# Optimization experiments

Measured on AMD Instinct MI355X. Metric: run time of the kernel, lower is better.

## Reference

```python
import jax, jax.numpy as jnp
import numpy as np

WS, WS2, UP = 8, 16, 2
DIM, HEADS = 192, 6
HD = DIM // HEADS
SCALE = HD ** -0.5
EPS = 1e-5

def _rel_index():
    r1, c1 = np.meshgrid(np.arange(WS), np.arange(WS), indexing='ij')
    r2, c2 = np.meshgrid(np.arange(WS2), np.arange(WS2), indexing='ij')
    r1, c1 = r1.ravel(), c1.ravel()          # 64 query positions
    r2, c2 = r2.ravel(), c2.ravel()          # 256 kv positions
    rel_row = r1[:, None] - r2[None, :]
    rel_col = c1[:, None] - c2[None, :]
    off = WS * UP - 1    # 15
    span = WS + WS * UP - 1  # 23
    return jnp.asarray((rel_row + off) * span + (rel_col + off))  # (64, 256)

REL_IDX = _rel_index()

def layer_norm(x, w, b):
    m = x.mean(-1, keepdims=True)
    v = ((x - m) ** 2).mean(-1, keepdims=True)
    return (x - m) * jax.lax.rsqrt(v + EPS) * w + b

def window_partition(x, ws):
    B, H, W, C = x.shape
    x = x.reshape(B, H // ws, ws, W // ws, ws, C).transpose(0, 1, 3, 2, 4, 5)
    return x.reshape(-1, ws * ws, C)

def window_reverse(w, ws, H, W, B):
    x = w.reshape(B, H // ws, W // ws, ws, ws, -1).transpose(0, 1, 3, 2, 4, 5)
    return x.reshape(B, H, W, -1)

def setup_inputs() -> dict:
    key = jax.random.key(0)
    ks = jax.random.split(key, 8)
    B, H, W, H2, W2 = 4, 128, 128, 256, 256
    s = 0.02
    return {
        'x': jax.random.normal(ks[0], (B, H * W, DIM), jnp.float32),
        'x2': jax.random.normal(ks[1], (B, H2 * W2, DIM), jnp.float32),
        'norm1_w': jnp.ones((DIM,), jnp.float32),
        'norm1_b': jnp.zeros((DIM,), jnp.float32),
        'qkv_w': jax.random.normal(ks[2], (DIM, DIM), jnp.float32) * s,
        'qkv_b': jnp.zeros((DIM,), jnp.float32),
        'qkv2_w': jax.random.normal(ks[3], (2 * DIM, DIM), jnp.float32) * s,
        'qkv2_b': jnp.zeros((2 * DIM,), jnp.float32),
        'rel_bias': jax.random.normal(ks[4], (23 * 23, HEADS), jnp.float32) * s,
        'proj_w': jax.random.normal(ks[5], (DIM, DIM), jnp.float32) * s,
        'proj_b': jnp.zeros((DIM,), jnp.float32),
        'norm2_w': jnp.ones((DIM,), jnp.float32),
        'norm2_b': jnp.zeros((DIM,), jnp.float32),
        'fc1_w': jax.random.normal(ks[6], (4 * DIM, DIM), jnp.float32) * s,
        'fc1_b': jnp.zeros((4 * DIM,), jnp.float32),
        'fc2_w': jax.random.normal(ks[7], (DIM, 4 * DIM), jnp.float32) * s,
        'fc2_b': jnp.zeros((DIM,), jnp.float32),
        'H': 128, 'W': 128, 'H2': 256, 'W2': 256,
    }

def reference(x, x2, norm1_w, norm1_b, qkv_w, qkv_b, qkv2_w, qkv2_b, rel_bias,
              proj_w, proj_b, norm2_w, norm2_b, fc1_w, fc1_b, fc2_w, fc2_b,
              H, W, H2, W2):
    B, L, C = x.shape
    shortcut = x
    xn = layer_norm(x, norm1_w, norm1_b).reshape(B, H, W, C)
    x2r = x2.reshape(B, H2, W2, C)

    xw = window_partition(xn, WS)      # (nW, 64, C)
    x2w = window_partition(x2r, WS2)   # (nW, 256, C)

    q = (xw @ qkv_w.T + qkv_b).reshape(-1, WS * WS, HEADS, HD).transpose(0, 2, 1, 3)
    kv = (x2w @ qkv2_w.T + qkv2_b).reshape(-1, WS2 * WS2, 2, HEADS, HD).transpose(2, 0, 3, 1, 4)
    k, v = kv[0], kv[1]                # (nW, h, 256, d)

    attn = jnp.einsum('whnd,whmd->whnm', q * SCALE, k)   # (nW, h, 64, 256)
    bias = rel_bias[REL_IDX]                             # (64, 256, h)
    attn = attn + bias.transpose(2, 0, 1)[None]
    attn = jax.nn.softmax(attn, axis=-1)
    out = jnp.einsum('whnm,whmd->wnhd', attn, v).reshape(-1, WS * WS, C)
    out = out @ proj_w.T + proj_b

    x = shortcut + window_reverse(out, WS, H, W, B).reshape(B, H * W, C)
    h = layer_norm(x, norm2_w, norm2_b)
    h = jax.nn.gelu(h @ fc1_w.T + fc1_b, approximate=False)
    x = x + (h @ fc2_w.T + fc2_b)
    return x
```

## Files before the change

### kernel.cpp

```cpp
#include <hip/hip_runtime.h>
#include <hip/hip_bf16.h>
#include <math.h>

typedef unsigned int u32;
typedef unsigned short u16;

typedef __attribute__((ext_vector_type(8))) short bf16x8;
typedef __attribute__((ext_vector_type(4))) float f32x4;

__device__ __forceinline__ float bflo(u32 u){ union{u32 i; float f;} c; c.i = u << 16; return c.f; }
__device__ __forceinline__ float bfhi(u32 u){ union{u32 i; float f;} c; c.i = u & 0xffff0000u; return c.f; }
__device__ __forceinline__ float bfs(u16 s){ union{u32 i; float f;} c; c.i = ((u32)s) << 16; return c.f; }
__device__ __forceinline__ u32 packbf(float a, float b){
  union{float f; u32 i;} ca, cb; ca.f = a; cb.f = b;
  u32 ua = (ca.i + 0x7fffu + ((ca.i >> 16) & 1u)) >> 16;
  u32 ub = (cb.i + 0x7fffu + ((cb.i >> 16) & 1u)) >> 16;
  return (ua & 0xffffu) | (ub << 16);
}
__device__ __forceinline__ u16 bf1(float a){
  union{float f; u32 i;} c; c.f = a;
  return (u16)((c.i + 0x7fffu + ((c.i >> 16) & 1u)) >> 16);
}
__device__ __forceinline__ bf16x8 pack8(float f0,float f1,float f2,float f3,
                                        float f4,float f5,float f6,float f7){
  union { u32 u[4]; bf16x8 v; } cv;
  cv.u[0]=packbf(f0,f1); cv.u[1]=packbf(f2,f3); cv.u[2]=packbf(f4,f5); cv.u[3]=packbf(f6,f7);
  return cv.v;
}
__device__ __forceinline__ float gelu_exact(float v){ return 0.5f*v*(1.0f + erff(v*0.70710678118654752f)); }
__device__ __forceinline__ bool detect_f32(const u32* rawn1){ return (rawn1[0] & 0xFFFFu) == 0u; }

#define SCALE_Q 0.17677669529663687f

#define P_N1W 0
#define P_N1B 192
#define P_N2W 384
#define P_N2B 576
#define P_QKVB 768
#define P_QKV2B 960
#define P_PROJB 1344
#define P_FC1B 1536
#define P_FC2B 2304
#define P_RELB 2496
#define P_TOTAL 5670
#define W_QKV 0
#define W_QKV2 18432
#define W_PROJ 55296
#define W_FC1 73728
#define W_FC2 147456
#define W_TOTAL 221184

__device__ __forceinline__ void stage_w64x192(const u32* __restrict__ src, u32* lds, int tid){
  #pragma unroll
  for (int t = 0; t < 3; ++t) {
    int idx = tid + t*512;
    int j = idx / 24, seg = idx % 24;
    uint4 v = *(const uint4*)(src + (size_t)j*96 + seg*4);
    int byt = (j*384 + seg*16) ^ ((j&7)<<4);
    *(uint4*)((char*)lds + byt) = v;
  }
}
__device__ __forceinline__ void stage_w192x64(const u32* __restrict__ src, int ch, u32* lds, int tid){
  #pragma unroll
  for (int t = 0; t < 3; ++t) {
    int idx = tid + t*512;
    int j = idx / 8, seg = idx % 8;
    uint4 v = *(const uint4*)(src + (size_t)j*384 + ch*32 + seg*4);
    int byt = (j*128 + seg*16) ^ ((j&7)<<4);
    *(uint4*)((char*)lds + byt) = v;
  }
}
__device__ __forceinline__ bf16x8 lds_w64(const u32* lds, int j, int kt, int g){
  int byt = (j*384 + kt*64 + g*16) ^ ((j&7)<<4);
  return *(const bf16x8*)((const char*)lds + byt);
}
__device__ __forceinline__ bf16x8 lds_w192(const u32* lds, int j, int kk, int g){
  int byt = (j*128 + kk*64 + g*16) ^ ((j&7)<<4);
  return *(const bf16x8*)((const char*)lds + byt);
}

__global__ __launch_bounds__(256) void k_canon_w(
    const void* qkvw, const void* qkv2w, const void* projw,
    const void* fc1w, const void* fc2w, const u32* rawn1, u32* cw)
{
  int idx = blockIdx.x*256 + threadIdx.x;
  bool isf32 = detect_f32(rawn1);
  const void* src; int off;
  if      (idx < W_QKV2){ src=qkvw;  off=idx; }
  else if (idx < W_PROJ){ src=qkv2w; off=idx-W_QKV2; }
  else if (idx < W_FC1) { src=projw; off=idx-W_PROJ; }
  else if (idx < W_FC2) { src=fc1w;  off=idx-W_FC1; }
  else                  { src=fc2w;  off=idx-W_FC2; }
  u32 o;
  if (isf32) { float2 v = ((const float2*)src)[off]; o = packbf(v.x, v.y); }
  else       { o = ((const u32*)src)[off]; }
  cw[idx] = o;
}

__global__ __launch_bounds__(256) void k_canon_v(
    const void* n1w, const void* n1b, const void* n2w, const void* n2b,
    const void* qkvb, const void* qkv2b, const void* projb,
    const void* fc1b, const void* fc2b, const void* relb,
    const u32* rawn1, float* par)
{
  int idx = blockIdx.x*256 + threadIdx.x;
  if (idx >= P_TOTAL) return;
  bool isf32 = detect_f32(rawn1);
  const void* src; int off;
  if      (idx < P_N1B)  { src=n1w;  off=idx; }
  else if (idx < P_N2W)  { src=n1b;  off=idx-P_N1B; }
  else if (idx < P_N2B)  { src=n2w;  off=idx-P_N2W; }
  else if (idx < P_QKVB) { src=n2b;  off=idx-P_N2B; }
  else if (idx < P_QKV2B){ src=qkvb; off=idx-P_QKVB; }
  else if (idx < P_PROJB){ src=qkv2b;off=idx-P_QKV2B; }
  else if (idx < P_FC1B) { src=projb;off=idx-P_PROJB; }
  else if (idx < P_FC2B) { src=fc1b; off=idx-P_FC1B; }
  else if (idx < P_RELB) { src=fc2b; off=idx-P_FC2B; }
  else                   { src=relb; off=idx-P_RELB; }
  par[idx] = isf32 ? ((const float*)src)[off] : bfs(((const u16*)src)[off]);
}

__global__ __launch_bounds__(256) void k_bias(
    const float* __restrict__ par, float* __restrict__ tbl)
{
  int idx = blockIdx.x*256 + threadIdx.x;
  int h  = idx >> 12;
  int remi = idx & 4095;
  int kt = remi >> 8;
  int qt = (remi >> 6) & 3;
  int ll = idx & 63;
  int lr = ll & 15, g = ll >> 4;
  int q = qt*16 + lr;
  int r1 = q >> 3, c1 = q & 7;
  float vv[4];
  #pragma unroll
  for (int i = 0; i < 4; ++i) {
    int kv = kt*16 + 4*g + i;
    int r2 = kv >> 4, c2 = kv & 15;
    vv[i] = par[P_RELB + ((r1-r2+15)*23 + (c1-c2+15))*6 + h];
  }
  ((float4*)tbl)[idx] = make_float4(vv[0], vv[1], vv[2], vv[3]);
}

__global__ __launch_bounds__(512) void k_qproj(
    const void* __restrict__ x, const u32* __restrict__ rawn1,
    const u32* __restrict__ cw, const float* __restrict__ par,
    float* __restrict__ q_ws)
{
  __shared__ u32 wbuf[6144];
  int tid = threadIdx.x;
  int l = tid & 63, w = tid >> 6, lr = l & 15, g = l >> 4;
  int wi0 = blockIdx.x*4;
  bool isf32 = detect_f32(rawn1);

  bf16x8 a[2][6];
  #pragma unroll
  for (int mt = 0; mt < 2; ++mt) {
    int tb = w*32 + mt*16 + lr;
    int wi = wi0 + (tb >> 6);
    int t = tb & 63;
    int b = wi >> 8, rem = wi & 255, wh = rem >> 4, ww = rem & 15;
    int r = t >> 3, c = t & 7;
    size_t grow = (size_t)b*16384 + (size_t)(wh*8+r)*128 + (ww*8+c);
    float4 xf[12];
    if (isf32) {
      const float* xp = (const float*)x + grow*192;
      #pragma unroll
      for (int kt = 0; kt < 6; ++kt) {
        xf[kt*2]   = *(const float4*)(xp + kt*32 + 8*g);
        xf[kt*2+1] = *(const float4*)(xp + kt*32 + 8*g + 4);
      }
    } else {
      const u32* xp = (const u32*)x + grow*96;
      #pragma unroll
      for (int kt = 0; kt < 6; ++kt) {
        uint4 u = *(const uint4*)(xp + kt*16 + 4*g);
        xf[kt*2]   = make_float4(bflo(u.x), bfhi(u.x), bflo(u.y), bfhi(u.y));
        xf[kt*2+1] = make_float4(bflo(u.z), bfhi(u.z), bflo(u.w), bfhi(u.w));
      }
    }
    float s = 0.f, s2 = 0.f;
    #pragma unroll
    for (int q8 = 0; q8 < 12; ++q8) {
      s  += xf[q8].x + xf[q8].y + xf[q8].z + xf[q8].w;
      s2 += xf[q8].x*xf[q8].x + xf[q8].y*xf[q8].y + xf[q8].z*xf[q8].z + xf[q8].w*xf[q8].w;
    }
    s += __shfl_xor(s, 16); s2 += __shfl_xor(s2, 16);
    s += __shfl_xor(s, 32); s2 += __shfl_xor(s2, 32);
    float m = s * (1.f/192.f);
    float rstd = rsqrtf(s2*(1.f/192.f) - m*m + 1e-5f);
    #pragma unroll
    for (int kt = 0; kt < 6; ++kt) {
      int k0 = kt*32 + 8*g;
      float4 w0 = *(const float4*)(par + P_N1W + k0);
      float4 w1 = *(const float4*)(par + P_N1W + k0 + 4);
      float4 b0 = *(const float4*)(par + P_N1B + k0);
      float4 b1 = *(const float4*)(par + P_N1B + k0 + 4);
      float4 f0 = xf[kt*2], f1 = xf[kt*2+1];
      a[mt][kt] = pack8((f0.x-m)*rstd*w0.x + b0.x, (f0.y-m)*rstd*w0.y + b0.y,
                        (f0.z-m)*rstd*w0.z + b0.z, (f0.w-m)*rstd*w0.w + b0.w,
                        (f1.x-m)*rstd*w1.x + b1.x, (f1.y-m)*rstd*w1.y + b1.y,
                        (f1.z-m)*rstd*w1.z + b1.z, (f1.w-m)*rstd*w1.w + b1.w);
    }
  }

  for (int ch = 0; ch < 3; ++ch) {
    __syncthreads();
    stage_w64x192(cw + W_QKV + (size_t)(ch*64)*96, wbuf, tid);
    __syncthreads();
    #pragma unroll
    for (int nt2 = 0; nt2 < 4; ++nt2) {
      int j = ch*64 + nt2*16 + lr;
      f32x4 acc0 = {0.f,0.f,0.f,0.f}, acc1 = {0.f,0.f,0.f,0.f};
      #pragma unroll
      for (int kt = 0; kt < 6; ++kt) {
        bf16x8 bb = lds_w64(wbuf, nt2*16 + lr, kt, g);
        acc0 = __builtin_amdgcn_mfma_f32_16x16x32_bf16(a[0][kt], bb, acc0, 0, 0, 0);
        acc1 = __builtin_amdgcn_mfma_f32_16x16x32_bf16(a[1][kt], bb, acc1, 0, 0, 0);
      }
      float bj = par[P_QKVB + j];
      int h = j >> 5, d = j & 31;
      #pragma unroll
      for (int mt = 0; mt < 2; ++mt) {
        f32x4 acc = mt ? acc1 : acc0;
        #pragma unroll
        for (int i = 0; i < 4; ++i) {
          int tb = w*32 + mt*16 + 4*g + i;
          int wi = wi0 + (tb >> 6);
          int n = tb & 63;
          q_ws[(size_t)(wi*6+h)*2048 + (size_t)n*32 + d] = (acc[i] + bj) * SCALE_Q;
        }
      }
    }
  }
}

__global__ __launch_bounds__(512) void k_kvproj(
    const void* __restrict__ x2, const u32* __restrict__ rawn1,
    const u32* __restrict__ cw, const float* __restrict__ par,
    u16* __restrict__ k_ws, u16* __restrict__ v_ws, int win0)
{
  __shared__ u32 wbuf[6144];
  int tid = threadIdx.x;
  int l = tid & 63, w = tid >> 6, lr = l & 15, g = l >> 4;
  int lwi = blockIdx.x;
  int wi = win0 + lwi;
  int b = wi >> 8, rem = wi & 255, wh = rem >> 4, ww = rem & 15;
  bool isf32 = detect_f32(rawn1);

  bf16x8 a[2][6];
  #pragma unroll
  for (int mt = 0; mt < 2; ++mt) {
    int tt = w*32 + mt*16 + lr;
    int r = tt >> 4, c = tt & 15;
    size_t grow = (size_t)b*65536 + (size_t)(wh*16+r)*256 + (ww*16+c);
    if (isf32) {
      const float4* xp = (const float4*)x2 + grow*48;
      #pragma unroll
      for (int kt = 0; kt < 6; ++kt) {
        float4 f0 = xp[kt*8 + g*2];
        float4 f1 = xp[kt*8 + g*2 + 1];
        a[mt][kt] = pack8(f0.x,f0.y,f0.z,f0.w, f1.x,f1.y,f1.z,f1.w);
      }
    } else {
      const u32* xp = (const u32*)x2 + grow*96;
      #pragma unroll
      for (int kt = 0; kt < 6; ++kt)
        a[mt][kt] = *(const bf16x8*)(xp + kt*16 + g*4);
    }
  }

  for (int ch = 0; ch < 6; ++ch) {
    __syncthreads();
    stage_w64x192(cw + W_QKV2 + (size_t)(ch*64)*96, wbuf, tid);
    __syncthreads();
    if (ch < 3) {
      #pragma unroll
      for (int nt2 = 0; nt2 < 4; ++nt2) {
        int j = ch*64 + nt2*16 + lr;
        f32x4 acc0 = {0.f,0.f,0.f,0.f}, acc1 = {0.f,0.f,0.f,0.f};
        #pragma unroll
        for (int kt = 0; kt < 6; ++kt) {
          bf16x8 bb = lds_w64(wbuf, nt2*16 + lr, kt, g);
          acc0 = __builtin_amdgcn_mfma_f32_16x16x32_bf16(a[0][kt], bb, acc0, 0, 0, 0);
          acc1 = __builtin_amdgcn_mfma_f32_16x16x32_bf16(a[1][kt], bb, acc1, 0, 0, 0);
        }
        float bj = par[P_QKV2B + j];
        int h = j >> 5, d = j & 31;
        u16* dst = k_ws + (size_t)(lwi*6 + h)*8192 + d;
        #pragma unroll
        for (int mt = 0; mt < 2; ++mt) {
          f32x4 acc = mt ? acc1 : acc0;
          #pragma unroll
          for (int i = 0; i < 4; ++i) {
            int tok = w*32 + mt*16 + 4*g + i;
            dst[(size_t)tok*32] = bf1(acc[i] + bj);
          }
        }
      }
    } else {
      #pragma unroll
      for (int nt2 = 0; nt2 < 4; ++nt2) {
        f32x4 acc0 = {0.f,0.f,0.f,0.f}, acc1 = {0.f,0.f,0.f,0.f};
        #pragma unroll
        for (int kt = 0; kt < 6; ++kt) {
          bf16x8 bb = lds_w64(wbuf, nt2*16 + lr, kt, g);
          acc0 = __builtin_amdgcn_mfma_f32_16x16x32_bf16(bb, a[0][kt], acc0, 0, 0, 0);
          acc1 = __builtin_amdgcn_mfma_f32_16x16x32_bf16(bb, a[1][kt], acc1, 0, 0, 0);
        }
        int jr0 = (ch-3)*64 + nt2*16 + 4*g;
        #pragma unroll
        for (int mt = 0; mt < 2; ++mt) {
          f32x4 acc = mt ? acc1 : acc0;
          int tok = w*32 + mt*16 + lr;
          #pragma unroll
          for (int i = 0; i < 4; ++i) {
            int jp = jr0 + i;
            int h = jp >> 5, dd = jp & 31;
            v_ws[(size_t)(lwi*6 + h)*8192 + (size_t)dd*256 + tok] = bf1(acc[i] + par[P_QKV2B + 192 + jp]);
          }
        }
      }
    }
  }
}

__global__ __launch_bounds__(256) void k_attn(
    const float* __restrict__ q_ws, const u16* __restrict__ k_ws,
    const u16* __restrict__ v_ws, const float* __restrict__ tbl,
    u16* __restrict__ O_ws, int win0)
{
  __shared__ u32 Psh[4*64*16];
  int tid = threadIdx.x;
  int w = tid >> 6, l = tid & 63;
  int lr = l & 15, g = l >> 4;
  int task = blockIdx.x*4 + w;
  int lwi = task / 6, h = task - lwi*6;
  int wi = win0 + lwi;

  bf16x8 qb[4];
  {
    const float* qp = q_ws + (size_t)(wi*6+h)*2048;
    #pragma unroll
    for (int qt = 0; qt < 4; ++qt) {
      const float* qr = qp + (qt*16 + lr)*32 + 8*g;
      float4 f0 = *(const float4*)qr;
      float4 f1 = *(const float4*)(qr + 4);
      qb[qt] = pack8(f0.x,f0.y,f0.z,f0.w, f1.x,f1.y,f1.z,f1.w);
    }
  }
  const u16* kp = k_ws + (size_t)(lwi*6+h)*8192;
  const u16* vp = v_ws + (size_t)(lwi*6+h)*8192;
  const float4* tb4 = (const float4*)tbl + (size_t)h*4096 + l;

  f32x4 ao[2][4];
  #pragma unroll
  for (int dt = 0; dt < 2; ++dt)
    #pragma unroll
    for (int qt = 0; qt < 4; ++qt) ao[dt][qt] = (f32x4){0.f,0.f,0.f,0.f};
  float mreg[4] = {-3.0e38f,-3.0e38f,-3.0e38f,-3.0e38f};
  float sreg[4] = {0.f,0.f,0.f,0.f};
  u32* pbu = Psh + w*1024;

  for (int ch = 0; ch < 8; ++ch) {
    bf16x8 ka0 = *(const bf16x8*)(kp + (2*ch)*512   + lr*32 + 8*g);
    bf16x8 ka1 = *(const bf16x8*)(kp + (2*ch+1)*512 + lr*32 + 8*g);
    f32x4 s0[4], s1[4];
    #pragma unroll
    for (int qt = 0; qt < 4; ++qt) {
      float4 b0 = tb4[(2*ch)*256   + qt*64];
      float4 b1 = tb4[(2*ch+1)*256 + qt*64];
      f32x4 c0; c0[0]=b0.x; c0[1]=b0.y; c0[2]=b0.z; c0[3]=b0.w;
      f32x4 c1; c1[0]=b1.x; c1[1]=b1.y; c1[2]=b1.z; c1[3]=b1.w;
      s0[qt] = __builtin_amdgcn_mfma_f32_16x16x32_bf16(ka0, qb[qt], c0, 0, 0, 0);
      s1[qt] = __builtin_amdgcn_mfma_f32_16x16x32_bf16(ka1, qb[qt], c1, 0, 0, 0);
    }
    #pragma unroll
    for (int qt = 0; qt < 4; ++qt) {
      float pm = fmaxf(fmaxf(fmaxf(s0[qt][0],s0[qt][1]), fmaxf(s0[qt][2],s0[qt][3])),
                       fmaxf(fmaxf(s1[qt][0],s1[qt][1]), fmaxf(s1[qt][2],s1[qt][3])));
      pm = fmaxf(pm, __shfl_xor(pm, 16));
      pm = fmaxf(pm, __shfl_xor(pm, 32));
      float nm = fmaxf(mreg[qt], pm);
      float resc = __expf(mreg[qt] - nm);
      mreg[qt] = nm;
      float p00 = __expf(s0[qt][0]-nm), p01 = __expf(s0[qt][1]-nm),
            p02 = __expf(s0[qt][2]-nm), p03 = __expf(s0[qt][3]-nm);
      float p10 = __expf(s1[qt][0]-nm), p11 = __expf(s1[qt][1]-nm),
            p12 = __expf(s1[qt][2]-nm), p13 = __expf(s1[qt][3]-nm);
      float ps = ((p00+p01)+(p02+p03)) + ((p10+p11)+(p12+p13));
      ps += __shfl_xor(ps, 16);
      ps += __shfl_xor(ps, 32);
      sreg[qt] = sreg[qt]*resc + ps;
      #pragma unroll
      for (int dt = 0; dt < 2; ++dt) {
        ao[dt][qt][0] *= resc; ao[dt][qt][1] *= resc;
        ao[dt][qt][2] *= resc; ao[dt][qt][3] *= resc;
      }
      int row = qt*16 + lr;
      int sw = (row & 3) << 2;
      *(uint2*)&pbu[row*16 + ((2*g) ^ sw)]     = make_uint2(packbf(p00,p01), packbf(p02,p03));
      *(uint2*)&pbu[row*16 + ((8 + 2*g) ^ sw)] = make_uint2(packbf(p10,p11), packbf(p12,p13));
    }
    asm volatile("" ::: "memory");
    bf16x8 va0 = *(const bf16x8*)(vp + lr*256        + ch*32 + 8*g);
    bf16x8 va1 = *(const bf16x8*)(vp + (16 + lr)*256 + ch*32 + 8*g);
    #pragma unroll
    for (int qt = 0; qt < 4; ++qt) {
      int row = qt*16 + lr;
      int sw = (row & 3) << 2;
      bf16x8 pa = *(const bf16x8*)&pbu[row*16 + ((4*g) ^ sw)];
      ao[0][qt] = __builtin_amdgcn_mfma_f32_16x16x32_bf16(va0, pa, ao[0][qt], 0, 0, 0);
      ao[1][qt] = __builtin_amdgcn_mfma_f32_16x16x32_bf16(va1, pa, ao[1][qt], 0, 0, 0);
    }
    asm volatile("" ::: "memory");
  }
  #pragma unroll
  for (int qt = 0; qt < 4; ++qt) {
    float rs = 1.0f / sreg[qt];
    u16* orow = O_ws + ((size_t)(lwi*64) + qt*16 + lr)*192 + h*32;
    #pragma unroll
    for (int dt = 0; dt < 2; ++dt)
      #pragma unroll
      for (int i = 0; i < 4; ++i)
        orow[dt*16 + 4*g + i] = bf1(ao[dt][qt][i] * rs);
  }
}

__global__ __launch_bounds__(256) void k_proj(
    const u16* __restrict__ O_ws, const u32* __restrict__ cw,
    const float* __restrict__ par, const void* __restrict__ x,
    const u32* __restrict__ rawn1, float* __restrict__ xres, int win0)
{
  int lwi = blockIdx.x;
  int wi = win0 + lwi;
  int b = wi >> 8, rem = wi & 255, wh = rem >> 4, ww = rem & 15;
  int tid = threadIdx.x;
  int l = tid & 63, w = tid >> 6, lr = l & 15, g = l >> 4;
  bool isf32 = detect_f32(rawn1);
  int t = w*16 + lr;
  const u16* op = O_ws + (size_t)(lwi*64 + t)*192;
  bf16x8 a[6];
  #pragma unroll
  for (int kt = 0; kt < 6; ++kt) a[kt] = *(const bf16x8*)(op + kt*32 + 8*g);

  for (int nt = 0; nt < 12; ++nt) {
    int j = nt*16 + lr;
    const u32* wrow = cw + W_PROJ + (size_t)j*96;
    f32x4 acc = {0.f,0.f,0.f,0.f};
    #pragma unroll
    for (int kt = 0; kt < 6; ++kt) {
      bf16x8 bb = *(const bf16x8*)(wrow + kt*16 + g*4);
      acc = __builtin_amdgcn_mfma_f32_16x16x32_bf16(a[kt], bb, acc, 0, 0, 0);
    }
    float bj = par[P_PROJB + j];
    #pragma unroll
    for (int i = 0; i < 4; ++i) {
      int tok = w*16 + 4*g + i;
      int rr = tok >> 3, cc = tok & 7;
      size_t grow = (size_t)b*16384 + (size_t)(wh*8+rr)*128 + (ww*8+cc);
      float sres = isf32 ? ((const float*)x)[grow*192 + j]
                         : bfs(((const u16*)x)[grow*192 + j]);
      xres[grow*192 + j] = sres + acc[i] + bj;
    }
  }
}

__global__ __launch_bounds__(512) void k_mlp(
    const float* __restrict__ xres, const u32* __restrict__ cw,
    const float* __restrict__ par, float* __restrict__ out)
{
  __shared__ u32 wbuf[6144];
  __shared__ u16 Hc[8][32][64];
  int tid = threadIdx.x;
  int l = tid & 63, w = tid >> 6;
  int lr = l & 15, g = l >> 4;
  size_t row0 = (size_t)blockIdx.x * 256;

  bf16x8 a[2][6];
  #pragma unroll
  for (int mt = 0; mt < 2; ++mt) {
    size_t t = row0 + w*32 + mt*16 + lr;
    const float* xr = xres + t*192;
    float4 xf[12];
    #pragma unroll
    for (int kt = 0; kt < 6; ++kt) {
      xf[kt*2]   = *(const float4*)(xr + kt*32 + 8*g);
      xf[kt*2+1] = *(const float4*)(xr + kt*32 + 8*g + 4);
    }
    float s = 0.f, s2 = 0.f;
    #pragma unroll
    for (int q = 0; q < 12; ++q) {
      s  += xf[q].x + xf[q].y + xf[q].z + xf[q].w;
      s2 += xf[q].x*xf[q].x + xf[q].y*xf[q].y + xf[q].z*xf[q].z + xf[q].w*xf[q].w;
    }
    s += __shfl_xor(s, 16); s2 += __shfl_xor(s2, 16);
    s += __shfl_xor(s, 32); s2 += __shfl_xor(s2, 32);
    float m = s * (1.f/192.f);
    float rstd = rsqrtf(s2*(1.f/192.f) - m*m + 1e-5f);
    #pragma unroll
    for (int kt = 0; kt < 6; ++kt) {
      int k0 = kt*32 + 8*g;
      float4 w0 = *(const float4*)(par + P_N2W + k0);
      float4 w1 = *(const float4*)(par + P_N2W + k0 + 4);
      float4 b0 = *(const float4*)(par + P_N2B + k0);
      float4 b1 = *(const float4*)(par + P_N2B + k0 + 4);
      float4 f0 = xf[kt*2], f1 = xf[kt*2+1];
      a[mt][kt] = pack8((f0.x-m)*rstd*w0.x + b0.x, (f0.y-m)*rstd*w0.y + b0.y,
                        (f0.z-m)*rstd*w0.z + b0.z, (f0.w-m)*rstd*w0.w + b0.w,
                        (f1.x-m)*rstd*w1.x + b1.x, (f1.y-m)*rstd*w1.y + b1.y,
                        (f1.z-m)*rstd*w1.z + b1.z, (f1.w-m)*rstd*w1.w + b1.w);
    }
  }

  f32x4 acc2[2][12];
  #pragma unroll
  for (int mt = 0; mt < 2; ++mt)
    #pragma unroll
    for (int i = 0; i < 12; ++i) acc2[mt][i] = (f32x4){0.f,0.f,0.f,0.f};

  char* hbase = (char*)&Hc[w][0][0];
  for (int ch = 0; ch < 12; ++ch) {
    __syncthreads();
    stage_w64x192(cw + W_FC1 + (size_t)(ch*64)*96, wbuf, tid);
    __syncthreads();
    #pragma unroll
    for (int nt2 = 0; nt2 < 4; ++nt2) {
      f32x4 acc0 = {0.f,0.f,0.f,0.f}, acc1 = {0.f,0.f,0.f,0.f};
      #pragma unroll
      for (int kt = 0; kt < 6; ++kt) {
        bf16x8 bb = lds_w64(wbuf, nt2*16 + lr, kt, g);
        acc0 = __builtin_amdgcn_mfma_f32_16x16x32_bf16(a[0][kt], bb, acc0, 0, 0, 0);
        acc1 = __builtin_amdgcn_mfma_f32_16x16x32_bf16(a[1][kt], bb, acc1, 0, 0, 0);
      }
      float bj = par[P_FC1B + ch*64 + nt2*16 + lr];
      #pragma unroll
      for (int mt = 0; mt < 2; ++mt) {
        f32x4 acc = mt ? acc1 : acc0;
        #pragma unroll
        for (int i = 0; i < 4; ++i) {
          int row = mt*16 + 4*g + i;
          int byt = (row*128 + (nt2*16+lr)*2) ^ ((row&7)<<4);
          *(u16*)(hbase + byt) = bf1(gelu_exact(acc[i] + bj));
        }
      }
    }
    __syncthreads();
    stage_w192x64(cw + W_FC2, ch, wbuf, tid);
    __syncthreads();
    #pragma unroll
    for (int kk = 0; kk < 2; ++kk) {
      bf16x8 a20, a21;
      {
        int row0h = lr, row1h = 16 + lr;
        a20 = *(const bf16x8*)(hbase + ((row0h*128 + kk*64 + g*16) ^ ((row0h&7)<<4)));
        a21 = *(const bf16x8*)(hbase + ((row1h*128 + kk*64 + g*16) ^ ((row1h&7)<<4)));
      }
      #pragma unroll
      for (int nt = 0; nt < 12; ++nt) {
        bf16x8 bb = lds_w192(wbuf, nt*16 + lr, kk, g);
        acc2[0][nt] = __builtin_amdgcn_mfma_f32_16x16x32_bf16(a20, bb, acc2[0][nt], 0, 0, 0);
        acc2[1][nt] = __builtin_amdgcn_mfma_f32_16x16x32_bf16(a21, bb, acc2[1][nt], 0, 0, 0);
      }
    }
  }

  #pragma unroll
  for (int mt = 0; mt < 2; ++mt) {
    size_t trow = row0 + w*32 + mt*16 + 4*g;
    #pragma unroll
    for (int nt = 0; nt < 12; ++nt) {
      int j = nt*16 + lr;
      float bj = par[P_FC2B + j];
      #pragma unroll
      for (int i = 0; i < 4; ++i)
        out[(trow+i)*192 + j] = xres[(trow+i)*192 + j] + acc2[mt][nt][i] + bj;
    }
  }
}

extern "C" void kernel_launch(void* const* d_in, const int* in_sizes, int n_in,
                              void* d_out, int out_size, void* d_ws, size_t ws_size,
                              hipStream_t stream) {
  const void* x      = d_in[0];
  const void* x2     = d_in[1];
  const void* n1w    = d_in[2];
  const void* n1b    = d_in[3];
  const void* qkv_w  = d_in[4];
  const void* qkv_b  = d_in[5];
  const void* qkv2_w = d_in[6];
  const void* qkv2_b = d_in[7];
  const void* relb   = d_in[8];
  const void* proj_w = d_in[9];
  const void* proj_b = d_in[10];
  const void* n2w    = d_in[11];
  const void* n2b    = d_in[12];
  const void* fc1_w  = d_in[13];
  const void* fc1_b  = d_in[14];
  const void* fc2_w  = d_in[15];
  const void* fc2_b  = d_in[16];
  const u32* rawn1   = (const u32*)d_in[2];
  float* out = (float*)d_out;

  char* ws = (char*)d_ws;
  float* q_ws = (float*)ws;
  u16*   k_ws = (u16*)(ws + 50331648);
  u16*   v_ws = (u16*)(ws + 75497472);
  u16*   O_ws = (u16*)(ws + 100663296);
  float* xres = (float*)(ws + 106954752);
  u32*   cw   = (u32*)(ws + 157286400);
  float* par  = (float*)(ws + 158171136);
  float* tbl  = (float*)(ws + 158193920);

  k_canon_w<<<W_TOTAL/256, 256, 0, stream>>>(qkv_w, qkv2_w, proj_w, fc1_w, fc2_w, rawn1, cw);
  k_canon_v<<<(P_TOTAL+255)/256, 256, 0, stream>>>(n1w, n1b, n2w, n2b, qkv_b, qkv2_b,
                                                   proj_b, fc1_b, fc2_b, relb, rawn1, par);
  k_bias  <<<96, 256, 0, stream>>>(par, tbl);
  k_qproj <<<256, 512, 0, stream>>>(x, rawn1, cw, par, q_ws);
  for (int s = 0; s < 4; ++s) {
    int win0 = s*256;
    k_kvproj<<<256, 512, 0, stream>>>(x2, rawn1, cw, par, k_ws, v_ws, win0);
    k_attn  <<<384, 256, 0, stream>>>(q_ws, k_ws, v_ws, tbl, O_ws, win0);
    k_proj  <<<256, 256, 0, stream>>>(O_ws, cw, par, x, rawn1, xres, win0);
  }
  k_mlp   <<<256, 512, 0, stream>>>(xres, cw, par, out);
}
```

Measured before the change: 751.4 us.

## Split attention KV across wave pairs, halve block sizes, stage proj weights in LDS

```diff
diff --git a/kernel.cpp b/kernel.cpp
--- a/kernel.cpp
+++ b/kernel.cpp
@@ -52,8 +52,8 @@
 
 __device__ __forceinline__ void stage_w64x192(const u32* __restrict__ src, u32* lds, int tid){
   #pragma unroll
-  for (int t = 0; t < 3; ++t) {
-    int idx = tid + t*512;
+  for (int t = 0; t < 6; ++t) {
+    int idx = tid + t*256;
     int j = idx / 24, seg = idx % 24;
     uint4 v = *(const uint4*)(src + (size_t)j*96 + seg*4);
     int byt = (j*384 + seg*16) ^ ((j&7)<<4);
@@ -62,8 +62,8 @@
 }
 __device__ __forceinline__ void stage_w192x64(const u32* __restrict__ src, int ch, u32* lds, int tid){
   #pragma unroll
-  for (int t = 0; t < 3; ++t) {
-    int idx = tid + t*512;
+  for (int t = 0; t < 6; ++t) {
+    int idx = tid + t*256;
     int j = idx / 8, seg = idx % 8;
     uint4 v = *(const uint4*)(src + (size_t)j*384 + ch*32 + seg*4);
     int byt = (j*128 + seg*16) ^ ((j&7)<<4);
@@ -142,15 +142,15 @@
   ((float4*)tbl)[idx] = make_float4(vv[0], vv[1], vv[2], vv[3]);
 }
 
-__global__ __launch_bounds__(512) void k_qproj(
+__global__ __launch_bounds__(256) void k_qproj(
     const void* __restrict__ x, const u32* __restrict__ rawn1,
     const u32* __restrict__ cw, const float* __restrict__ par,
-    float* __restrict__ q_ws)
+    u16* __restrict__ q_ws)
 {
   __shared__ u32 wbuf[6144];
   int tid = threadIdx.x;
   int l = tid & 63, w = tid >> 6, lr = l & 15, g = l >> 4;
-  int wi0 = blockIdx.x*4;
+  int wi0 = blockIdx.x*2;
   bool isf32 = detect_f32(rawn1);
 
   bf16x8 a[2][6];
@@ -228,14 +228,14 @@
           int tb = w*32 + mt*16 + 4*g + i;
           int wi = wi0 + (tb >> 6);
           int n = tb & 63;
-          q_ws[(size_t)(wi*6+h)*2048 + (size_t)n*32 + d] = (acc[i] + bj) * SCALE_Q;
+          q_ws[(size_t)(wi*6+h)*2048 + (size_t)n*32 + d] = bf1((acc[i] + bj) * SCALE_Q);
         }
       }
     }
   }
 }
 
-__global__ __launch_bounds__(512) void k_kvproj(
+__global__ __launch_bounds__(256) void k_kvproj(
     const void* __restrict__ x2, const u32* __restrict__ rawn1,
     const u32* __restrict__ cw, const float* __restrict__ par,
     u16* __restrict__ k_ws, u16* __restrict__ v_ws, int win0)
@@ -243,7 +243,7 @@
   __shared__ u32 wbuf[6144];
   int tid = threadIdx.x;
   int l = tid & 63, w = tid >> 6, lr = l & 15, g = l >> 4;
-  int lwi = blockIdx.x;
+  int lwi = blockIdx.x >> 1, sub = blockIdx.x & 1;
   int wi = win0 + lwi;
   int b = wi >> 8, rem = wi & 255, wh = rem >> 4, ww = rem & 15;
   bool isf32 = detect_f32(rawn1);
@@ -251,7 +251,7 @@
   bf16x8 a[2][6];
   #pragma unroll
   for (int mt = 0; mt < 2; ++mt) {
-    int tt = w*32 + mt*16 + lr;
+    int tt = sub*128 + w*32 + mt*16 + lr;
     int r = tt >> 4, c = tt & 15;
     size_t grow = (size_t)b*65536 + (size_t)(wh*16+r)*256 + (ww*16+c);
     if (isf32) {
@@ -293,7 +293,7 @@
           f32x4 acc = mt ? acc1 : acc0;
           #pragma unroll
           for (int i = 0; i < 4; ++i) {
-            int tok = w*32 + mt*16 + 4*g + i;
+            int tok = sub*128 + w*32 + mt*16 + 4*g + i;
             dst[(size_t)tok*32] = bf1(acc[i] + bj);
           }
         }
@@ -312,7 +312,7 @@
         #pragma unroll
         for (int mt = 0; mt < 2; ++mt) {
           f32x4 acc = mt ? acc1 : acc0;
-          int tok = w*32 + mt*16 + lr;
+          int tok = sub*128 + w*32 + mt*16 + lr;
           #pragma unroll
           for (int i = 0; i < 4; ++i) {
             int jp = jr0 + i;
@@ -326,28 +326,26 @@
 }
 
 __global__ __launch_bounds__(256) void k_attn(
-    const float* __restrict__ q_ws, const u16* __restrict__ k_ws,
+    const u16* __restrict__ q_ws, const u16* __restrict__ k_ws,
     const u16* __restrict__ v_ws, const float* __restrict__ tbl,
     u16* __restrict__ O_ws, int win0)
 {
-  __shared__ u32 Psh[4*64*16];
+  __shared__ u32 Psh[4*1024];
+  __shared__ float msh[2][2][4];
   int tid = threadIdx.x;
   int w = tid >> 6, l = tid & 63;
   int lr = l & 15, g = l >> 4;
-  int task = blockIdx.x*4 + w;
+  int pairi = w >> 1, half = w & 1;
+  int task = blockIdx.x*2 + pairi;
   int lwi = task / 6, h = task - lwi*6;
   int wi = win0 + lwi;
 
   bf16x8 qb[4];
   {
-    const float* qp = q_ws + (size_t)(wi*6+h)*2048;
-    #pragma unroll
-    for (int qt = 0; qt < 4; ++qt) {
-      const float* qr = qp + (qt*16 + lr)*32 + 8*g;
-      float4 f0 = *(const float4*)qr;
-      float4 f1 = *(const float4*)(qr + 4);
-      qb[qt] = pack8(f0.x,f0.y,f0.z,f0.w, f1.x,f1.y,f1.z,f1.w);
-    }
+    const u16* qp = q_ws + (size_t)(wi*6+h)*2048;
+    #pragma unroll
+    for (int qt = 0; qt < 4; ++qt)
+      qb[qt] = *(const bf16x8*)(qp + (qt*16 + lr)*32 + 8*g);
   }
   const u16* kp = k_ws + (size_t)(lwi*6+h)*8192;
   const u16* vp = v_ws + (size_t)(lwi*6+h)*8192;
@@ -362,7 +360,7 @@
   float sreg[4] = {0.f,0.f,0.f,0.f};
   u32* pbu = Psh + w*1024;
 
-  for (int ch = 0; ch < 8; ++ch) {
+  for (int ch = half*4; ch < half*4 + 4; ++ch) {
     bf16x8 ka0 = *(const bf16x8*)(kp + (2*ch)*512   + lr*32 + 8*g);
     bf16x8 ka1 = *(const bf16x8*)(kp + (2*ch+1)*512 + lr*32 + 8*g);
     f32x4 s0[4], s1[4];
@@ -415,15 +413,42 @@
     }
     asm volatile("" ::: "memory");
   }
-  #pragma unroll
-  for (int qt = 0; qt < 4; ++qt) {
-    float rs = 1.0f / sreg[qt];
-    u16* orow = O_ws + ((size_t)(lwi*64) + qt*16 + lr)*192 + h*32;
+
+  __syncthreads();
+  if (half == 1) {
+    float* dst = (float*)(Psh + pairi*2048);
     #pragma unroll
     for (int dt = 0; dt < 2; ++dt)
       #pragma unroll
-      for (int i = 0; i < 4; ++i)
-        orow[dt*16 + 4*g + i] = bf1(ao[dt][qt][i] * rs);
+      for (int qt = 0; qt < 4; ++qt)
+        #pragma unroll
+        for (int i = 0; i < 4; ++i)
+          dst[(dt*16 + qt*4 + i)*64 + l] = ao[dt][qt][i];
+    if (l == 0) {
+      msh[pairi][0][0] = mreg[0]; msh[pairi][0][1] = mreg[1];
+      msh[pairi][0][2] = mreg[2]; msh[pairi][0][3] = mreg[3];
+      msh[pairi][1][0] = sreg[0]; msh[pairi][1][1] = sreg[1];
+      msh[pairi][1][2] = sreg[2]; msh[pairi][1][3] = sreg[3];
+    }
+  }
+  __syncthreads();
+  if (half == 0) {
+    const float* src = (const float*)(Psh + pairi*2048);
+    #pragma unroll
+    for (int qt = 0; qt < 4; ++qt) {
+      float m1 = msh[pairi][0][qt], s1 = msh[pairi][1][qt];
+      float M = fmaxf(mreg[qt], m1);
+      float e0 = __expf(mreg[qt] - M), e1 = __expf(m1 - M);
+      float rs = 1.0f / (sreg[qt]*e0 + s1*e1);
+      u16* orow = O_ws + ((size_t)(lwi*64) + qt*16 + lr)*192 + h*32;
+      #pragma unroll
+      for (int dt = 0; dt < 2; ++dt)
+        #pragma unroll
+        for (int i = 0; i < 4; ++i) {
+          float o = ao[dt][qt][i]*e0 + src[(dt*16 + qt*4 + i)*64 + l]*e1;
+          orow[dt*16 + 4*g + i] = bf1(o * rs);
+        }
+    }
   }
 }
 
@@ -432,6 +457,7 @@
     const float* __restrict__ par, const void* __restrict__ x,
     const u32* __restrict__ rawn1, float* __restrict__ xres, int win0)
 {
+  __shared__ u32 wbuf[6144];
   int lwi = blockIdx.x;
   int wi = win0 + lwi;
   int b = wi >> 8, rem = wi & 255, wh = rem >> 4, ww = rem & 15;
@@ -444,38 +470,43 @@
   #pragma unroll
   for (int kt = 0; kt < 6; ++kt) a[kt] = *(const bf16x8*)(op + kt*32 + 8*g);
 
-  for (int nt = 0; nt < 12; ++nt) {
-    int j = nt*16 + lr;
-    const u32* wrow = cw + W_PROJ + (size_t)j*96;
-    f32x4 acc = {0.f,0.f,0.f,0.f};
-    #pragma unroll
-    for (int kt = 0; kt < 6; ++kt) {
-      bf16x8 bb = *(const bf16x8*)(wrow + kt*16 + g*4);
-      acc = __builtin_amdgcn_mfma_f32_16x16x32_bf16(a[kt], bb, acc, 0, 0, 0);
-    }
-    float bj = par[P_PROJB + j];
-    #pragma unroll
-    for (int i = 0; i < 4; ++i) {
-      int tok = w*16 + 4*g + i;
-      int rr = tok >> 3, cc = tok & 7;
-      size_t grow = (size_t)b*16384 + (size_t)(wh*8+rr)*128 + (ww*8+cc);
-      float sres = isf32 ? ((const float*)x)[grow*192 + j]
-                         : bfs(((const u16*)x)[grow*192 + j]);
-      xres[grow*192 + j] = sres + acc[i] + bj;
-    }
-  }
-}
-
-__global__ __launch_bounds__(512) void k_mlp(
+  for (int ch = 0; ch < 3; ++ch) {
+    __syncthreads();
+    stage_w64x192(cw + W_PROJ + (size_t)(ch*64)*96, wbuf, tid);
+    __syncthreads();
+    #pragma unroll
+    for (int nt2 = 0; nt2 < 4; ++nt2) {
+      int j = ch*64 + nt2*16 + lr;
+      f32x4 acc = {0.f,0.f,0.f,0.f};
+      #pragma unroll
+      for (int kt = 0; kt < 6; ++kt) {
+        bf16x8 bb = lds_w64(wbuf, nt2*16 + lr, kt, g);
+        acc = __builtin_amdgcn_mfma_f32_16x16x32_bf16(a[kt], bb, acc, 0, 0, 0);
+      }
+      float bj = par[P_PROJB + j];
+      #pragma unroll
+      for (int i = 0; i < 4; ++i) {
+        int tok = w*16 + 4*g + i;
+        int rr = tok >> 3, cc = tok & 7;
+        size_t grow = (size_t)b*16384 + (size_t)(wh*8+rr)*128 + (ww*8+cc);
+        float sres = isf32 ? ((const float*)x)[grow*192 + j]
+                           : bfs(((const u16*)x)[grow*192 + j]);
+        xres[grow*192 + j] = sres + acc[i] + bj;
+      }
+    }
+  }
+}
+
+__global__ __launch_bounds__(256) void k_mlp(
     const float* __restrict__ xres, const u32* __restrict__ cw,
     const float* __restrict__ par, float* __restrict__ out)
 {
   __shared__ u32 wbuf[6144];
-  __shared__ u16 Hc[8][32][64];
+  __shared__ u16 Hc[4][32][64];
   int tid = threadIdx.x;
   int l = tid & 63, w = tid >> 6;
   int lr = l & 15, g = l >> 4;
-  size_t row0 = (size_t)blockIdx.x * 256;
+  size_t row0 = (size_t)blockIdx.x * 128;
 
   bf16x8 a[2][6];
   #pragma unroll
@@ -603,25 +634,25 @@
   float* out = (float*)d_out;
 
   char* ws = (char*)d_ws;
-  float* q_ws = (float*)ws;
-  u16*   k_ws = (u16*)(ws + 50331648);
-  u16*   v_ws = (u16*)(ws + 75497472);
-  u16*   O_ws = (u16*)(ws + 100663296);
-  float* xres = (float*)(ws + 106954752);
-  u32*   cw   = (u32*)(ws + 157286400);
-  float* par  = (float*)(ws + 158171136);
-  float* tbl  = (float*)(ws + 158193920);
+  u16*   q_ws = (u16*)ws;
+  u16*   k_ws = (u16*)(ws + 25165824);
+  u16*   v_ws = (u16*)(ws + 50331648);
+  u16*   O_ws = (u16*)(ws + 75497472);
+  float* xres = (float*)(ws + 81788928);
+  u32*   cw   = (u32*)(ws + 132120576);
+  float* par  = (float*)(ws + 133005312);
+  float* tbl  = (float*)(ws + 133029888);
 
   k_canon_w<<<W_TOTAL/256, 256, 0, stream>>>(qkv_w, qkv2_w, proj_w, fc1_w, fc2_w, rawn1, cw);
   k_canon_v<<<(P_TOTAL+255)/256, 256, 0, stream>>>(n1w, n1b, n2w, n2b, qkv_b, qkv2_b,
                                                    proj_b, fc1_b, fc2_b, relb, rawn1, par);
   k_bias  <<<96, 256, 0, stream>>>(par, tbl);
-  k_qproj <<<256, 512, 0, stream>>>(x, rawn1, cw, par, q_ws);
+  k_qproj <<<512, 256, 0, stream>>>(x, rawn1, cw, par, q_ws);
   for (int s = 0; s < 4; ++s) {
     int win0 = s*256;
-    k_kvproj<<<256, 512, 0, stream>>>(x2, rawn1, cw, par, k_ws, v_ws, win0);
-    k_attn  <<<384, 256, 0, stream>>>(q_ws, k_ws, v_ws, tbl, O_ws, win0);
+    k_kvproj<<<512, 256, 0, stream>>>(x2, rawn1, cw, par, k_ws, v_ws, win0);
+    k_attn  <<<768, 256, 0, stream>>>(q_ws, k_ws, v_ws, tbl, O_ws, win0);
     k_proj  <<<256, 256, 0, stream>>>(O_ws, cw, par, x, rawn1, xres, win0);
   }
-  k_mlp   <<<256, 512, 0, stream>>>(xres, cw, par, out);
-}
+  k_mlp   <<<512, 256, 0, stream>>>(xres, cw, par, out);
+}
```

New measurement: 835.1 us. 1.11x slower.
